# Kernel tuning notes

Measured on AMD Instinct MI355X. Metric: run time of the kernel, lower is better.

Reference implementation:

```python
import math
import jax, jax.numpy as jnp
import numpy as np

EPS = 1e-5
DIM_E = 448
DIM_H = 64
TOTAL = DIM_E + DIM_H  # 512
C = 1.0


def _project(x, c, margin=1e-3):
    sqrt_c = jnp.sqrt(c)
    norm = jnp.maximum(jnp.linalg.norm(x, axis=-1, keepdims=True), EPS)
    scale = jnp.minimum(((1.0 - margin) / sqrt_c) / norm, 1.0)
    return x * scale


def _mobius_add(x, y, c):
    x2 = jnp.sum(x * x, axis=-1, keepdims=True)
    y2 = jnp.sum(y * y, axis=-1, keepdims=True)
    xy = jnp.sum(x * y, axis=-1, keepdims=True)
    num = (1.0 + 2.0 * c * xy + c * y2) * x + (1.0 - c * x2) * y
    den = jnp.maximum(1.0 + 2.0 * c * xy + c * c * x2 * y2, EPS)
    return _project(num / den, c)


def _exp0(v, c):
    sqrt_c = jnp.sqrt(c)
    norm = jnp.maximum(jnp.linalg.norm(v, axis=-1, keepdims=True), EPS)
    return _project(jnp.tanh(sqrt_c * norm) * v / (sqrt_c * norm), c)


def _dist(x, y, c):
    # x, y broadcast to [B,S,S,dim_h]; returns [B,S,S]
    sqrt_c = jnp.sqrt(c)
    diff = _mobius_add(-x, y, c)
    norm = jnp.minimum(jnp.linalg.norm(diff, axis=-1), (1.0 - 1e-5) / sqrt_c)
    return (2.0 / sqrt_c) * jnp.arctanh(jnp.minimum(sqrt_c * norm, 1.0 - 1e-5))


def setup_inputs() -> dict:
    key = jax.random.key(0)
    ks = jax.random.split(key, 10)
    B, S = 1, 1024
    s = 1.0 / math.sqrt(TOTAL)
    inp = {
        "x": jax.random.normal(ks[0], (B, S, TOTAL), jnp.float32),
        "wq": jax.random.uniform(ks[1], (TOTAL, TOTAL), jnp.float32, -s, s),
        "bq": jax.random.uniform(ks[2], (TOTAL,), jnp.float32, -s, s),
        "wk": jax.random.uniform(ks[3], (TOTAL, TOTAL), jnp.float32, -s, s),
        "bk": jax.random.uniform(ks[4], (TOTAL,), jnp.float32, -s, s),
        "wv": jax.random.uniform(ks[5], (TOTAL, TOTAL), jnp.float32, -s, s),
        "bv": jax.random.uniform(ks[6], (TOTAL,), jnp.float32, -s, s),
        "wo": jax.random.uniform(ks[7], (TOTAL, TOTAL), jnp.float32, -s, s),
        "bo": jax.random.uniform(ks[8], (TOTAL,), jnp.float32, -s, s),
        "alpha_unconstrained": jnp.float32(0.0),
    }
    return inp


def reference(x, wq, bq, wk, bk, wv, bv, wo, bo, alpha_unconstrained):
    q = x @ wq.T + bq
    k = x @ wk.T + bk
    v = x @ wv.T + bv
    qe, qh = q[..., :DIM_E], q[..., DIM_E:]
    ke, kh = k[..., :DIM_E], k[..., DIM_E:]
    # Euclidean squared distance [B,S,S] via GEMM expansion
    qn = jnp.sum(qe * qe, axis=-1)  # [B,S]
    kn = jnp.sum(ke * ke, axis=-1)  # [B,S]
    d_e = qn[:, :, None] + kn[:, None, :] - 2.0 * jnp.einsum("bsd,btd->bst", qe, ke)
    # Hyperbolic distance on Poincare ball
    qh_h = _exp0(qh, C)
    kh_h = _exp0(kh, C)
    d_h = _dist(qh_h[:, :, None, :], kh_h[:, None, :, :], C)  # [B,S,S]
    alpha = jax.nn.softplus(alpha_unconstrained)
    dist = d_e + alpha * d_h * d_h
    logits = jnp.clip(-dist / math.sqrt(float(TOTAL)), -50.0, 0.0)
    attn = jax.nn.softmax(logits, axis=-1)
    out = jnp.einsum("bst,btd->bsd", attn, v)
    return out @ wo.T + bo
```

## Files before the change

kernel.cpp:

```cpp
#include <hip/hip_runtime.h>

#define S_LEN 1024
#define D_TOT 512
#define D_E   448

typedef short bf16x8 __attribute__((ext_vector_type(8)));
typedef float f32x4  __attribute__((ext_vector_type(4)));
typedef unsigned short u16;

__device__ __forceinline__ float frcp(float x) {
  float r; asm("v_rcp_f32 %0, %1" : "=v"(r) : "v"(x)); return r;
}

__device__ __forceinline__ float wave_sum64(float v) {
#pragma unroll
  for (int o = 32; o > 0; o >>= 1) v += __shfl_xor(v, o);
  return v;
}

__device__ __forceinline__ u16 bf16rne(float f) {
  unsigned u = __builtin_bit_cast(unsigned, f);
  return (u16)((u + 0x7fffu + ((u >> 16) & 1u)) >> 16);
}

__device__ __forceinline__ uint4 rne8(float4 a, float4 b) {
  uint4 h;
  h.x = (unsigned)bf16rne(a.x) | ((unsigned)bf16rne(a.y)<<16);
  h.y = (unsigned)bf16rne(a.z) | ((unsigned)bf16rne(a.w)<<16);
  h.z = (unsigned)bf16rne(b.x) | ((unsigned)bf16rne(b.y)<<16);
  h.w = (unsigned)bf16rne(b.z) | ((unsigned)bf16rne(b.w)<<16);
  return h;
}

#define MFMA1(ACC)                                                                              \
  _Pragma("unroll") for (int i_ = 0; i_ < 2; ++i_)                                              \
  _Pragma("unroll") for (int j_ = 0; j_ < 2; ++j_)                                              \
    ACC[i_][j_] = __builtin_amdgcn_mfma_f32_16x16x32_bf16(fAh[i_], fBh[j_], ACC[i_][j_],0,0,0);

__global__ __launch_bounds__(512,4) void qkv_mfma(
    const float* __restrict__ x,
    const float* __restrict__ wq, const float* __restrict__ bq,
    const float* __restrict__ wk, const float* __restrict__ bk,
    const float* __restrict__ wv, const float* __restrict__ bv,
    u16* __restrict__ Qch, u16* __restrict__ Kch, u16* __restrict__ vTh,
    float* __restrict__ qnpart, float* __restrict__ knpart,
    float* __restrict__ uh2a, float* __restrict__ vh2a)
{
  __shared__ __align__(16) u16 stage[2][10240];
  float* fbuf = (float*)stage;
  const int z = blockIdx.z;
  const float* W; const float* bias;
  if (z == 0)      { W = wq; bias = bq; }
  else if (z == 1) { W = wk; bias = bk; }
  else             { W = wv; bias = bv; }
  const int mBase = blockIdx.y << 6, nBase = blockIdx.x << 6;
  const int t = threadIdx.x, lane = t & 63, wave = t >> 6;
  const int kg = t >> 8, sub = t & 255;
  const int srow = sub >> 2, scol = (sub & 3) << 3;
  const int kgw = wave >> 2, wr = (wave >> 1) & 1, wc = wave & 1;

  const float* Ag = x + (size_t)(mBase + srow) * D_TOT + scol + kg * 256;
  const float* Bg = W + (size_t)(nBase + srow) * D_TOT + scol + kg * 256;

  const int sb = kg * 5120 + srow * 40 + scol;
  const int fa = kgw * 5120 + (wr * 32 + (lane & 15)) * 40 + ((lane >> 4) << 3);
  const int fb = kgw * 5120 + 2560 + (wc * 32 + (lane & 15)) * 40 + ((lane >> 4) << 3);

  float4 a0 = *(const float4*)Ag, a1 = *(const float4*)(Ag + 4);
  float4 b0 = *(const float4*)Bg, b1 = *(const float4*)(Bg + 4);
  *(uint4*)&stage[0][sb       ] = rne8(a0,a1);
  *(uint4*)&stage[0][sb + 2560] = rne8(b0,b1);
  a0 = *(const float4*)(Ag + 32); a1 = *(const float4*)(Ag + 36);
  b0 = *(const float4*)(Bg + 32); b1 = *(const float4*)(Bg + 36);

  f32x4 zero = {0.f,0.f,0.f,0.f};
  f32x4 acc[2][2] = {{zero,zero},{zero,zero}};
#pragma unroll
  for (int r = 0; r < 8; ++r) {
    __syncthreads();
    const u16* bufr = stage[r & 1];
    bf16x8 fAh[2], fBh[2];
#pragma unroll
    for (int i = 0; i < 2; ++i) {
      fAh[i] = *(const bf16x8*)&bufr[fa + i*640];
      fBh[i] = *(const bf16x8*)&bufr[fb + i*640];
    }
    if (r + 1 < 8) {
      u16* bufw = stage[(r + 1) & 1];
      *(uint4*)&bufw[sb       ] = rne8(a0,a1);
      *(uint4*)&bufw[sb + 2560] = rne8(b0,b1);
      if (r + 2 < 8) {
        const int o = (r + 2) * 32;
        a0 = *(const float4*)(Ag + o); a1 = *(const float4*)(Ag + o + 4);
        b0 = *(const float4*)(Bg + o); b1 = *(const float4*)(Bg + o + 4);
      }
    }
    MFMA1(acc);
  }

  __syncthreads();
  {
    const int r0 = wr*32 + ((lane>>4)<<2);
    const int c0 = wc*32 + (lane&15);
#pragma unroll
    for (int i = 0; i < 2; ++i)
#pragma unroll
      for (int j = 0; j < 2; ++j)
#pragma unroll
        for (int g = 0; g < 4; ++g)
          fbuf[kgw*4352 + (r0 + i*16 + g)*68 + c0 + j*16] = acc[i][j][g];
  }
  __syncthreads();
  const int erow = wave << 3;
  float val[8];
  {
    const float b = bias[nBase + lane];
#pragma unroll
    for (int r = 0; r < 8; ++r)
      val[r] = fbuf[(erow+r)*68 + lane] + fbuf[4352 + (erow+r)*68 + lane] + b;
  }

  if (z == 2) {
    u16 hh[8];
#pragma unroll
    for (int r = 0; r < 8; ++r) hh[r] = bf16rne(val[r]);
    const size_t off = (size_t)(nBase + lane) * S_LEN + mBase + erow;
    ushort4 p0{hh[0],hh[1],hh[2],hh[3]}, p1{hh[4],hh[5],hh[6],hh[7]};
    *(ushort4*)(vTh + off) = p0; *(ushort4*)(vTh + off + 4) = p1;
  } else {
    u16* Ch = z ? Kch : Qch;
    float* np_ = z ? knpart : qnpart;
    float* u2a = z ? vh2a  : uh2a;
    if (blockIdx.x < 7) {
#pragma unroll
      for (int r = 0; r < 8; ++r) {
        const int s = mBase + erow + r;
        Ch[(size_t)s*D_TOT + nBase + lane] = bf16rne(val[r]);
        float p = wave_sum64(val[r]*val[r]);
        if (lane == 0) np_[s*8 + blockIdx.x] = p;
      }
    } else {
#pragma unroll
      for (int r = 0; r < 8; ++r) {
        const int s = mBase + erow + r;
        float n2 = wave_sum64(val[r]*val[r]);
        float nn = sqrtf(n2);
        float n  = fmaxf(nn, 1e-5f);
        float e2n = __expf(2.f*n);
        float th  = 1.f - 2.f*frcp(e2n + 1.f);
        float rn  = frcp(n);
        float pn  = th * nn * rn;
        float scale = fminf(0.999f * frcp(fmaxf(pn, 1e-5f)), 1.f);
        float u = th * rn * scale * val[r];
        float un = pn * scale;
        Ch[(size_t)s*D_TOT + nBase + lane] = bf16rne(u);
        if (lane == 0) u2a[s] = un*un;
      }
    }
  }
}

__global__ __launch_bounds__(512,4) void score_mfma(
    const u16* __restrict__ Qch, const u16* __restrict__ Kch,
    const float* __restrict__ qnpart, const float* __restrict__ knpart,
    const float* __restrict__ uh2a, const float* __restrict__ vh2a,
    const float* __restrict__ alpha_u,
    u16* __restrict__ Eh, float* __restrict__ rowpart)
{
  __shared__ __align__(16) char shm_[69632];
  __shared__ float rowscal[256];
  u16* stg = (u16*)shm_;
  float* fbuf = (float*)shm_;
  const int t = threadIdx.x, lane = t & 63, wave = t >> 6;
  const int mBase = blockIdx.y << 6, nBase = blockIdx.x << 6;
  if (t < 64) {
    float s_ = 0.f;
#pragma unroll
    for (int c = 0; c < 7; ++c) s_ += qnpart[(mBase+t)*8 + c];
    rowscal[t] = s_;
  } else if (t < 128) {
    float s_ = 0.f;
#pragma unroll
    for (int c = 0; c < 7; ++c) s_ += knpart[(nBase+t-64)*8 + c];
    rowscal[t] = s_;
  } else if (t < 192) rowscal[t] = uh2a[mBase + t - 128];
  else if (t < 256)   rowscal[t] = vh2a[nBase + t - 192];

  const int kg = t >> 8, sub = t & 255;
  const int srow = sub >> 2, scol = (sub & 3) << 3;
  const int kgw = wave >> 2, wr = (wave >> 1) & 1, wc = wave & 1;
  const u16* Agh = Qch + (size_t)(mBase+srow)*D_TOT + scol;
  const u16* Bgh = Kch + (size_t)(nBase+srow)*D_TOT + scol;

  const int sb  = kg * 5120 + srow * 40 + scol;
  const int fa  = kgw * 5120 + (wr * 32 + (lane & 15)) * 40 + ((lane >> 4) << 3);
  const int fbh = kgw * 5120 + 2560 + (wc * 32 + (lane & 15)) * 40 + ((lane >> 4) << 3);

  int kb = kg * 224;
  uint4 rAh = *(const uint4*)(Agh + kb);
  uint4 rBh = *(const uint4*)(Bgh + kb);
  *(uint4*)&stg[sb       ] = rAh;
  *(uint4*)&stg[sb + 2560] = rBh;
  kb = kg * 224 + 32;
  rAh = *(const uint4*)(Agh + kb);
  rBh = *(const uint4*)(Bgh + kb);

  f32x4 zero = {0.f,0.f,0.f,0.f};
  f32x4 accE[2][2] = {{zero,zero},{zero,zero}};
  f32x4 accH[2][2] = {{zero,zero},{zero,zero}};
#pragma unroll
  for (int r = 0; r < 8; ++r) {
    __syncthreads();
    const u16* bufr = stg + (r & 1) * 10240;
    bf16x8 fAh[2], fBh[2];
#pragma unroll
    for (int i = 0; i < 2; ++i) {
      fAh[i] = *(const bf16x8*)&bufr[fa  + i*640];
      fBh[i] = *(const bf16x8*)&bufr[fbh + i*640];
    }
    if (r + 1 < 8) {
      u16* bufw = stg + ((r + 1) & 1) * 10240;
      *(uint4*)&bufw[sb       ] = rAh;
      *(uint4*)&bufw[sb + 2560] = rBh;
      if (r + 2 < 8) {
        const int o = (r + 2 < 7) ? (kg*224 + (r+2)*32) : (448 + kg*32);
        rAh = *(const uint4*)(Agh + o);
        rBh = *(const uint4*)(Bgh + o);
      }
    }
    if (r < 7) { MFMA1(accE) } else { MFMA1(accH) }
  }

  __syncthreads();
  {
    const int r0 = wr*32 + ((lane>>4)<<2);
    const int c0 = wc*32 + (lane&15);
#pragma unroll
    for (int i = 0; i < 2; ++i)
#pragma unroll
      for (int j = 0; j < 2; ++j)
#pragma unroll
        for (int g = 0; g < 4; ++g) {
          fbuf[       kgw*4352 + (r0 + i*16 + g)*68 + c0 + j*16] = accE[i][j][g];
          fbuf[8704 + kgw*4352 + (r0 + i*16 + g)*68 + c0 + j*16] = accH[i][j][g];
        }
  }
  __syncthreads();
  const int erow = wave << 3;
  float eE[8], eH[8];
#pragma unroll
  for (int r = 0; r < 8; ++r) {
    eE[r] = fbuf[(erow+r)*68 + lane] + fbuf[4352 + (erow+r)*68 + lane];
    eH[r] = fbuf[8704 + (erow+r)*68 + lane] + fbuf[8704 + 4352 + (erow+r)*68 + lane];
  }

  const float alpha = __logf(1.f + __expf(alpha_u[0]));
  const float inv_s = 0.04419417382415922f;
  const float knl = rowscal[64 + lane], v2 = rowscal[192 + lane];
#pragma unroll
  for (int r = 0; r < 8; ++r) {
    const int s = mBase + erow + r;
    const float qns = rowscal[erow + r], u2 = rowscal[128 + erow + r];
    float de   = qns + knl - 2.f * eE[r];
    float dH   = eH[r];
    float Ac   = 1.f - 2.f*dH + v2;
    float Bc   = 1.f - u2;
    float num2 = Ac*Ac*u2 + Bc*Bc*v2 - 2.f*Ac*Bc*dH;
    float den  = fmaxf(1.f - 2.f*dH + u2*v2, 1e-5f);
    float frac = sqrtf(fmaxf(num2, 0.f)) * frcp(den);
    float nrm  = fminf(frac, 0.999f);
    float dh_  = __logf((1.f + nrm) * frcp(1.f - nrm));
    float dist = de + alpha * dh_ * dh_;
    float lg   = fminf(fmaxf(-dist * inv_s, -50.f), 0.f);
    float e    = __expf(lg);
    Eh[(size_t)s*S_LEN + nBase + lane] = bf16rne(e);
    float rs = wave_sum64(e);
    if (lane == 0) rowpart[s*16 + blockIdx.x] = rs;
  }
}

__global__ __launch_bounds__(512,4) void av_mfma(
    const u16* __restrict__ Eh, const u16* __restrict__ vTh,
    const float* __restrict__ rowpart,
    u16* __restrict__ out1h)
{
  __shared__ __align__(16) u16 stage[2][15360];
  __shared__ float rinvl[32];
  float* fbuf = (float*)stage;
  const int t = threadIdx.x, lane = t & 63, wave = t >> 6;
  const int mBase = blockIdx.y << 5, nBase = blockIdx.x << 6;
  if (t < 32) {
    float s_ = 0.f;
#pragma unroll
    for (int c = 0; c < 16; ++c) s_ += rowpart[(mBase+t)*16 + c];
    rinvl[t] = 1.f / s_;
  }
  const int kg = t >> 7, sub = t & 127;
  const int arow = sub >> 2, acol = (sub & 3) << 3;
  const int brow0 = sub >> 2, brow1 = 32 + (sub >> 2), bcol = (sub & 3) << 3;
  const int kgw = wave >> 1, wc = wave & 1;

  const u16* Ag = Eh  + (size_t)(mBase+arow)*S_LEN + kg*256 + acol;
  const u16* B0 = vTh + (size_t)(nBase+brow0)*S_LEN + kg*256 + bcol;
  const u16* B1 = vTh + (size_t)(nBase+brow1)*S_LEN + kg*256 + bcol;

  const int sA  = kg*3840 + arow*40 + acol;
  const int sB0 = kg*3840 + 1280 + brow0*40 + bcol;
  const int sB1 = kg*3840 + 1280 + brow1*40 + bcol;
  const int fa  = kgw*3840 + (lane&15)*40 + ((lane>>4)<<3);
  const int fb  = kgw*3840 + 1280 + (wc*32 + (lane&15))*40 + ((lane>>4)<<3);

  uint4 rA = *(const uint4*)Ag;
  uint4 rb0 = *(const uint4*)B0, rb1 = *(const uint4*)B1;
  *(uint4*)&stage[0][sA ] = rA;
  *(uint4*)&stage[0][sB0] = rb0; *(uint4*)&stage[0][sB1] = rb1;
  rA = *(const uint4*)(Ag + 32);
  rb0 = *(const uint4*)(B0 + 32); rb1 = *(const uint4*)(B1 + 32);

  f32x4 zero = {0.f,0.f,0.f,0.f};
  f32x4 acc[2][2] = {{zero,zero},{zero,zero}};
#pragma unroll
  for (int r = 0; r < 8; ++r) {
    __syncthreads();
    const u16* bufr = stage[r & 1];
    bf16x8 fAh[2], fBh[2];
#pragma unroll
    for (int i = 0; i < 2; ++i) {
      fAh[i] = *(const bf16x8*)&bufr[fa + i*640];
      fBh[i] = *(const bf16x8*)&bufr[fb + i*640];
    }
    if (r + 1 < 8) {
      u16* bufw = stage[(r + 1) & 1];
      *(uint4*)&bufw[sA ] = rA;
      *(uint4*)&bufw[sB0] = rb0; *(uint4*)&bufw[sB1] = rb1;
      if (r + 2 < 8) {
        const int o = (r + 2) * 32;
        rA = *(const uint4*)(Ag + o);
        rb0 = *(const uint4*)(B0 + o); rb1 = *(const uint4*)(B1 + o);
      }
    }
    MFMA1(acc);
  }

  __syncthreads();
  {
    const int r0 = (lane>>4)<<2;
    const int c0 = wc*32 + (lane&15);
#pragma unroll
    for (int i = 0; i < 2; ++i)
#pragma unroll
      for (int j = 0; j < 2; ++j)
#pragma unroll
        for (int g = 0; g < 4; ++g)
          fbuf[kgw*2176 + (r0 + i*16 + g)*68 + c0 + j*16] = acc[i][j][g];
  }
  __syncthreads();
  const int erow = wave << 2;
#pragma unroll
  for (int r = 0; r < 4; ++r) {
    const int row = erow + r;
    float e = fbuf[row*68 + lane] + fbuf[2176 + row*68 + lane]
            + fbuf[4352 + row*68 + lane] + fbuf[6528 + row*68 + lane];
    float v_ = e * rinvl[row];
    const int s = mBase + row;
    out1h[(size_t)s*D_TOT + nBase + lane] = bf16rne(v_);
  }
}

__global__ __launch_bounds__(512,4) void final_mfma(
    const u16* __restrict__ out1h,
    const float* __restrict__ wo, const float* __restrict__ bo,
    float* __restrict__ out)
{
  __shared__ __align__(16) u16 stage[2][15360];
  float* fbuf = (float*)stage;
  const int t = threadIdx.x, lane = t & 63, wave = t >> 6;
  const int mBase = blockIdx.y << 5, nBase = blockIdx.x << 6;
  const int kg = t >> 7, sub = t & 127;
  const int arow = sub >> 2, acol = (sub & 3) << 3;
  const int brow0 = sub >> 2, brow1 = 32 + (sub >> 2), bcol = (sub & 3) << 3;
  const int kgw = wave >> 1, wc = wave & 1;

  const u16*   Ag = out1h + (size_t)(mBase+arow)*D_TOT + kg*128 + acol;
  const float* B0 = wo + (size_t)(nBase+brow0)*D_TOT + kg*128 + bcol;
  const float* B1 = wo + (size_t)(nBase+brow1)*D_TOT + kg*128 + bcol;

  const int sA  = kg*3840 + arow*40 + acol;
  const int sB0 = kg*3840 + 1280 + brow0*40 + bcol;
  const int sB1 = kg*3840 + 1280 + brow1*40 + bcol;
  const int fa  = kgw*3840 + (lane&15)*40 + ((lane>>4)<<3);
  const int fb  = kgw*3840 + 1280 + (wc*32 + (lane&15))*40 + ((lane>>4)<<3);

  uint4 rA = *(const uint4*)Ag;
  float4 b00 = *(const float4*)B0, b01 = *(const float4*)(B0 + 4);
  float4 b10 = *(const float4*)B1, b11 = *(const float4*)(B1 + 4);
  *(uint4*)&stage[0][sA ] = rA;
  *(uint4*)&stage[0][sB0] = rne8(b00,b01);
  *(uint4*)&stage[0][sB1] = rne8(b10,b11);
  rA = *(const uint4*)(Ag + 32);
  b00 = *(const float4*)(B0 + 32); b01 = *(const float4*)(B0 + 36);
  b10 = *(const float4*)(B1 + 32); b11 = *(const float4*)(B1 + 36);

  f32x4 zero = {0.f,0.f,0.f,0.f};
  f32x4 acc[2][2] = {{zero,zero},{zero,zero}};
#pragma unroll
  for (int r = 0; r < 4; ++r) {
    __syncthreads();
    const u16* bufr = stage[r & 1];
    bf16x8 fAh[2], fBh[2];
#pragma unroll
    for (int i = 0; i < 2; ++i) {
      fAh[i] = *(const bf16x8*)&bufr[fa + i*640];
      fBh[i] = *(const bf16x8*)&bufr[fb + i*640];
    }
    if (r + 1 < 4) {
      u16* bufw = stage[(r + 1) & 1];
      *(uint4*)&bufw[sA ] = rA;
      *(uint4*)&bufw[sB0] = rne8(b00,b01);
      *(uint4*)&bufw[sB1] = rne8(b10,b11);
      if (r + 2 < 4) {
        const int o = (r + 2) * 32;
        rA = *(const uint4*)(Ag + o);
        b00 = *(const float4*)(B0 + o); b01 = *(const float4*)(B0 + o + 4);
        b10 = *(const float4*)(B1 + o); b11 = *(const float4*)(B1 + o + 4);
      }
    }
    MFMA1(acc);
  }

  __syncthreads();
  {
    const int r0 = (lane>>4)<<2;
    const int c0 = wc*32 + (lane&15);
#pragma unroll
    for (int i = 0; i < 2; ++i)
#pragma unroll
      for (int j = 0; j < 2; ++j)
#pragma unroll
        for (int g = 0; g < 4; ++g)
          fbuf[kgw*2176 + (r0 + i*16 + g)*68 + c0 + j*16] = acc[i][j][g];
  }
  __syncthreads();
  const int erow = wave << 2;
  const float b = bo[nBase + lane];
#pragma unroll
  for (int r = 0; r < 4; ++r) {
    const int row = erow + r;
    float e = fbuf[row*68 + lane] + fbuf[2176 + row*68 + lane]
            + fbuf[4352 + row*68 + lane] + fbuf[6528 + row*68 + lane];
    out[(size_t)(mBase+row)*D_TOT + nBase + lane] = e + b;
  }
}

extern "C" void kernel_launch(void* const* d_in, const int* in_sizes, int n_in,
                              void* d_out, int out_size, void* d_ws, size_t ws_size,
                              hipStream_t stream)
{
  const float* x   = (const float*)d_in[0];
  const float* wq  = (const float*)d_in[1];
  const float* bq  = (const float*)d_in[2];
  const float* wk  = (const float*)d_in[3];
  const float* bk  = (const float*)d_in[4];
  const float* wv  = (const float*)d_in[5];
  const float* bv  = (const float*)d_in[6];
  const float* wo  = (const float*)d_in[7];
  const float* bo  = (const float*)d_in[8];
  const float* alpha_u = (const float*)d_in[9];
  float* out = (float*)d_out;

  u16* U = (u16*)d_ws;
  u16* Qch   = U + 0;
  u16* Kch   = U + 524288;
  u16* vTh   = U + 1048576;
  u16* Eh    = U + 1572864;
  u16* out1h = U + 2621440;
  float* F = (float*)(U + 3145728);
  float* qnpart  = F;
  float* knpart  = F + 8192;
  float* uh2a    = F + 16384;
  float* vh2a    = F + 17408;
  float* rowpart = F + 18432;

  qkv_mfma<<<dim3(8,16,3), 512, 0, stream>>>(x, wq,bq, wk,bk, wv,bv,
      Qch, Kch, vTh, qnpart, knpart, uh2a, vh2a);
  score_mfma<<<dim3(16,16), 512, 0, stream>>>(Qch, Kch,
      qnpart, knpart, uh2a, vh2a, alpha_u, Eh, rowpart);
  av_mfma<<<dim3(8,32), 512, 0, stream>>>(Eh, vTh, rowpart, out1h);
  final_mfma<<<dim3(8,32), 512, 0, stream>>>(out1h, wo, bo, out);
}
```

Before: 34.59 us.

## Move V projection into score kernel to balance grid and overlap work

```diff
diff --git a/kernel.cpp b/kernel.cpp
--- a/kernel.cpp
+++ b/kernel.cpp
@@ -37,22 +37,19 @@
   _Pragma("unroll") for (int j_ = 0; j_ < 2; ++j_)                                              \
     ACC[i_][j_] = __builtin_amdgcn_mfma_f32_16x16x32_bf16(fAh[i_], fBh[j_], ACC[i_][j_],0,0,0);
 
-__global__ __launch_bounds__(512,4) void qkv_mfma(
+__global__ __launch_bounds__(512,4) void qk_mfma(
     const float* __restrict__ x,
     const float* __restrict__ wq, const float* __restrict__ bq,
     const float* __restrict__ wk, const float* __restrict__ bk,
-    const float* __restrict__ wv, const float* __restrict__ bv,
-    u16* __restrict__ Qch, u16* __restrict__ Kch, u16* __restrict__ vTh,
+    u16* __restrict__ Qch, u16* __restrict__ Kch,
     float* __restrict__ qnpart, float* __restrict__ knpart,
     float* __restrict__ uh2a, float* __restrict__ vh2a)
 {
   __shared__ __align__(16) u16 stage[2][10240];
   float* fbuf = (float*)stage;
   const int z = blockIdx.z;
-  const float* W; const float* bias;
-  if (z == 0)      { W = wq; bias = bq; }
-  else if (z == 1) { W = wk; bias = bk; }
-  else             { W = wv; bias = bv; }
+  const float* W    = z ? wk : wq;
+  const float* bias = z ? bk : bq;
   const int mBase = blockIdx.y << 6, nBase = blockIdx.x << 6;
   const int t = threadIdx.x, lane = t & 63, wave = t >> 6;
   const int kg = t >> 8, sub = t & 255;
@@ -120,162 +117,228 @@
       val[r] = fbuf[(erow+r)*68 + lane] + fbuf[4352 + (erow+r)*68 + lane] + b;
   }
 
-  if (z == 2) {
-    u16 hh[8];
-#pragma unroll
-    for (int r = 0; r < 8; ++r) hh[r] = bf16rne(val[r]);
-    const size_t off = (size_t)(nBase + lane) * S_LEN + mBase + erow;
-    ushort4 p0{hh[0],hh[1],hh[2],hh[3]}, p1{hh[4],hh[5],hh[6],hh[7]};
-    *(ushort4*)(vTh + off) = p0; *(ushort4*)(vTh + off + 4) = p1;
+  u16* Ch = z ? Kch : Qch;
+  float* np_ = z ? knpart : qnpart;
+  float* u2a = z ? vh2a  : uh2a;
+  if (blockIdx.x < 7) {
+#pragma unroll
+    for (int r = 0; r < 8; ++r) {
+      const int s = mBase + erow + r;
+      Ch[(size_t)s*D_TOT + nBase + lane] = bf16rne(val[r]);
+      float p = wave_sum64(val[r]*val[r]);
+      if (lane == 0) np_[s*8 + blockIdx.x] = p;
+    }
   } else {
-    u16* Ch = z ? Kch : Qch;
-    float* np_ = z ? knpart : qnpart;
-    float* u2a = z ? vh2a  : uh2a;
-    if (blockIdx.x < 7) {
-#pragma unroll
-      for (int r = 0; r < 8; ++r) {
-        const int s = mBase + erow + r;
-        Ch[(size_t)s*D_TOT + nBase + lane] = bf16rne(val[r]);
-        float p = wave_sum64(val[r]*val[r]);
-        if (lane == 0) np_[s*8 + blockIdx.x] = p;
-      }
-    } else {
-#pragma unroll
-      for (int r = 0; r < 8; ++r) {
-        const int s = mBase + erow + r;
-        float n2 = wave_sum64(val[r]*val[r]);
-        float nn = sqrtf(n2);
-        float n  = fmaxf(nn, 1e-5f);
-        float e2n = __expf(2.f*n);
-        float th  = 1.f - 2.f*frcp(e2n + 1.f);
-        float rn  = frcp(n);
-        float pn  = th * nn * rn;
-        float scale = fminf(0.999f * frcp(fmaxf(pn, 1e-5f)), 1.f);
-        float u = th * rn * scale * val[r];
-        float un = pn * scale;
-        Ch[(size_t)s*D_TOT + nBase + lane] = bf16rne(u);
-        if (lane == 0) u2a[s] = un*un;
-      }
-    }
-  }
-}
-
-__global__ __launch_bounds__(512,4) void score_mfma(
+#pragma unroll
+    for (int r = 0; r < 8; ++r) {
+      const int s = mBase + erow + r;
+      float n2 = wave_sum64(val[r]*val[r]);
+      float nn = sqrtf(n2);
+      float n  = fmaxf(nn, 1e-5f);
+      float e2n = __expf(2.f*n);
+      float th  = 1.f - 2.f*frcp(e2n + 1.f);
+      float rn  = frcp(n);
+      float pn  = th * nn * rn;
+      float scale = fminf(0.999f * frcp(fmaxf(pn, 1e-5f)), 1.f);
+      float u = th * rn * scale * val[r];
+      float un = pn * scale;
+      Ch[(size_t)s*D_TOT + nBase + lane] = bf16rne(u);
+      if (lane == 0) u2a[s] = un*un;
+    }
+  }
+}
+
+__global__ __launch_bounds__(512,4) void score_v(
     const u16* __restrict__ Qch, const u16* __restrict__ Kch,
     const float* __restrict__ qnpart, const float* __restrict__ knpart,
     const float* __restrict__ uh2a, const float* __restrict__ vh2a,
     const float* __restrict__ alpha_u,
-    u16* __restrict__ Eh, float* __restrict__ rowpart)
+    const float* __restrict__ x,
+    const float* __restrict__ wv, const float* __restrict__ bv,
+    u16* __restrict__ Eh, float* __restrict__ rowpart,
+    u16* __restrict__ vTh)
 {
   __shared__ __align__(16) char shm_[69632];
   __shared__ float rowscal[256];
   u16* stg = (u16*)shm_;
   float* fbuf = (float*)shm_;
+  const int bid = blockIdx.x;
   const int t = threadIdx.x, lane = t & 63, wave = t >> 6;
-  const int mBase = blockIdx.y << 6, nBase = blockIdx.x << 6;
-  if (t < 64) {
-    float s_ = 0.f;
-#pragma unroll
-    for (int c = 0; c < 7; ++c) s_ += qnpart[(mBase+t)*8 + c];
-    rowscal[t] = s_;
-  } else if (t < 128) {
-    float s_ = 0.f;
-#pragma unroll
-    for (int c = 0; c < 7; ++c) s_ += knpart[(nBase+t-64)*8 + c];
-    rowscal[t] = s_;
-  } else if (t < 192) rowscal[t] = uh2a[mBase + t - 128];
-  else if (t < 256)   rowscal[t] = vh2a[nBase + t - 192];
-
   const int kg = t >> 8, sub = t & 255;
   const int srow = sub >> 2, scol = (sub & 3) << 3;
   const int kgw = wave >> 2, wr = (wave >> 1) & 1, wc = wave & 1;
-  const u16* Agh = Qch + (size_t)(mBase+srow)*D_TOT + scol;
-  const u16* Bgh = Kch + (size_t)(nBase+srow)*D_TOT + scol;
-
-  const int sb  = kg * 5120 + srow * 40 + scol;
-  const int fa  = kgw * 5120 + (wr * 32 + (lane & 15)) * 40 + ((lane >> 4) << 3);
-  const int fbh = kgw * 5120 + 2560 + (wc * 32 + (lane & 15)) * 40 + ((lane >> 4) << 3);
-
-  int kb = kg * 224;
-  uint4 rAh = *(const uint4*)(Agh + kb);
-  uint4 rBh = *(const uint4*)(Bgh + kb);
-  *(uint4*)&stg[sb       ] = rAh;
-  *(uint4*)&stg[sb + 2560] = rBh;
-  kb = kg * 224 + 32;
-  rAh = *(const uint4*)(Agh + kb);
-  rBh = *(const uint4*)(Bgh + kb);
-
-  f32x4 zero = {0.f,0.f,0.f,0.f};
-  f32x4 accE[2][2] = {{zero,zero},{zero,zero}};
-  f32x4 accH[2][2] = {{zero,zero},{zero,zero}};
-#pragma unroll
-  for (int r = 0; r < 8; ++r) {
-    __syncthreads();
-    const u16* bufr = stg + (r & 1) * 10240;
-    bf16x8 fAh[2], fBh[2];
-#pragma unroll
-    for (int i = 0; i < 2; ++i) {
-      fAh[i] = *(const bf16x8*)&bufr[fa  + i*640];
-      fBh[i] = *(const bf16x8*)&bufr[fbh + i*640];
-    }
-    if (r + 1 < 8) {
-      u16* bufw = stg + ((r + 1) & 1) * 10240;
-      *(uint4*)&bufw[sb       ] = rAh;
-      *(uint4*)&bufw[sb + 2560] = rBh;
-      if (r + 2 < 8) {
-        const int o = (r + 2 < 7) ? (kg*224 + (r+2)*32) : (448 + kg*32);
-        rAh = *(const uint4*)(Agh + o);
-        rBh = *(const uint4*)(Bgh + o);
-      }
-    }
-    if (r < 7) { MFMA1(accE) } else { MFMA1(accH) }
-  }
-
-  __syncthreads();
-  {
-    const int r0 = wr*32 + ((lane>>4)<<2);
-    const int c0 = wc*32 + (lane&15);
-#pragma unroll
-    for (int i = 0; i < 2; ++i)
-#pragma unroll
-      for (int j = 0; j < 2; ++j)
-#pragma unroll
-        for (int g = 0; g < 4; ++g) {
-          fbuf[       kgw*4352 + (r0 + i*16 + g)*68 + c0 + j*16] = accE[i][j][g];
-          fbuf[8704 + kgw*4352 + (r0 + i*16 + g)*68 + c0 + j*16] = accH[i][j][g];
+
+  if (bid < 256) {
+    const int nx = bid & 15;
+    const int mBase = (bid >> 4) << 6, nBase = nx << 6;
+    if (t < 64) {
+      float s_ = 0.f;
+#pragma unroll
+      for (int c = 0; c < 7; ++c) s_ += qnpart[(mBase+t)*8 + c];
+      rowscal[t] = s_;
+    } else if (t < 128) {
+      float s_ = 0.f;
+#pragma unroll
+      for (int c = 0; c < 7; ++c) s_ += knpart[(nBase+t-64)*8 + c];
+      rowscal[t] = s_;
+    } else if (t < 192) rowscal[t] = uh2a[mBase + t - 128];
+    else if (t < 256)   rowscal[t] = vh2a[nBase + t - 192];
+
+    const u16* Agh = Qch + (size_t)(mBase+srow)*D_TOT + scol;
+    const u16* Bgh = Kch + (size_t)(nBase+srow)*D_TOT + scol;
+
+    const int sb  = kg * 5120 + srow * 40 + scol;
+    const int fa  = kgw * 5120 + (wr * 32 + (lane & 15)) * 40 + ((lane >> 4) << 3);
+    const int fbh = kgw * 5120 + 2560 + (wc * 32 + (lane & 15)) * 40 + ((lane >> 4) << 3);
+
+    int kb = kg * 224;
+    uint4 rAh = *(const uint4*)(Agh + kb);
+    uint4 rBh = *(const uint4*)(Bgh + kb);
+    *(uint4*)&stg[sb       ] = rAh;
+    *(uint4*)&stg[sb + 2560] = rBh;
+    kb = kg * 224 + 32;
+    rAh = *(const uint4*)(Agh + kb);
+    rBh = *(const uint4*)(Bgh + kb);
+
+    f32x4 zero = {0.f,0.f,0.f,0.f};
+    f32x4 accE[2][2] = {{zero,zero},{zero,zero}};
+    f32x4 accH[2][2] = {{zero,zero},{zero,zero}};
+#pragma unroll
+    for (int r = 0; r < 8; ++r) {
+      __syncthreads();
+      const u16* bufr = stg + (r & 1) * 10240;
+      bf16x8 fAh[2], fBh[2];
+#pragma unroll
+      for (int i = 0; i < 2; ++i) {
+        fAh[i] = *(const bf16x8*)&bufr[fa  + i*640];
+        fBh[i] = *(const bf16x8*)&bufr[fbh + i*640];
+      }
+      if (r + 1 < 8) {
+        u16* bufw = stg + ((r + 1) & 1) * 10240;
+        *(uint4*)&bufw[sb       ] = rAh;
+        *(uint4*)&bufw[sb + 2560] = rBh;
+        if (r + 2 < 8) {
+          const int o = (r + 2 < 7) ? (kg*224 + (r+2)*32) : (448 + kg*32);
+          rAh = *(const uint4*)(Agh + o);
+          rBh = *(const uint4*)(Bgh + o);
         }
-  }
-  __syncthreads();
-  const int erow = wave << 3;
-  float eE[8], eH[8];
-#pragma unroll
-  for (int r = 0; r < 8; ++r) {
-    eE[r] = fbuf[(erow+r)*68 + lane] + fbuf[4352 + (erow+r)*68 + lane];
-    eH[r] = fbuf[8704 + (erow+r)*68 + lane] + fbuf[8704 + 4352 + (erow+r)*68 + lane];
-  }
-
-  const float alpha = __logf(1.f + __expf(alpha_u[0]));
-  const float inv_s = 0.04419417382415922f;
-  const float knl = rowscal[64 + lane], v2 = rowscal[192 + lane];
-#pragma unroll
-  for (int r = 0; r < 8; ++r) {
-    const int s = mBase + erow + r;
-    const float qns = rowscal[erow + r], u2 = rowscal[128 + erow + r];
-    float de   = qns + knl - 2.f * eE[r];
-    float dH   = eH[r];
-    float Ac   = 1.f - 2.f*dH + v2;
-    float Bc   = 1.f - u2;
-    float num2 = Ac*Ac*u2 + Bc*Bc*v2 - 2.f*Ac*Bc*dH;
-    float den  = fmaxf(1.f - 2.f*dH + u2*v2, 1e-5f);
-    float frac = sqrtf(fmaxf(num2, 0.f)) * frcp(den);
-    float nrm  = fminf(frac, 0.999f);
-    float dh_  = __logf((1.f + nrm) * frcp(1.f - nrm));
-    float dist = de + alpha * dh_ * dh_;
-    float lg   = fminf(fmaxf(-dist * inv_s, -50.f), 0.f);
-    float e    = __expf(lg);
-    Eh[(size_t)s*S_LEN + nBase + lane] = bf16rne(e);
-    float rs = wave_sum64(e);
-    if (lane == 0) rowpart[s*16 + blockIdx.x] = rs;
+      }
+      if (r < 7) { MFMA1(accE) } else { MFMA1(accH) }
+    }
+
+    __syncthreads();
+    {
+      const int r0 = wr*32 + ((lane>>4)<<2);
+      const int c0 = wc*32 + (lane&15);
+#pragma unroll
+      for (int i = 0; i < 2; ++i)
+#pragma unroll
+        for (int j = 0; j < 2; ++j)
+#pragma unroll
+          for (int g = 0; g < 4; ++g) {
+            fbuf[       kgw*4352 + (r0 + i*16 + g)*68 + c0 + j*16] = accE[i][j][g];
+            fbuf[8704 + kgw*4352 + (r0 + i*16 + g)*68 + c0 + j*16] = accH[i][j][g];
+          }
+    }
+    __syncthreads();
+    const int erow = wave << 3;
+    float eE[8], eH[8];
+#pragma unroll
+    for (int r = 0; r < 8; ++r) {
+      eE[r] = fbuf[(erow+r)*68 + lane] + fbuf[4352 + (erow+r)*68 + lane];
+      eH[r] = fbuf[8704 + (erow+r)*68 + lane] + fbuf[8704 + 4352 + (erow+r)*68 + lane];
+    }
+
+    const float alpha = __logf(1.f + __expf(alpha_u[0]));
+    const float inv_s = 0.04419417382415922f;
+    const float knl = rowscal[64 + lane], v2 = rowscal[192 + lane];
+#pragma unroll
+    for (int r = 0; r < 8; ++r) {
+      const int s = mBase + erow + r;
+      const float qns = rowscal[erow + r], u2 = rowscal[128 + erow + r];
+      float de   = qns + knl - 2.f * eE[r];
+      float dH   = eH[r];
+      float Ac   = 1.f - 2.f*dH + v2;
+      float Bc   = 1.f - u2;
+      float num2 = Ac*Ac*u2 + Bc*Bc*v2 - 2.f*Ac*Bc*dH;
+      float den  = fmaxf(1.f - 2.f*dH + u2*v2, 1e-5f);
+      float frac = sqrtf(fmaxf(num2, 0.f)) * frcp(den);
+      float nrm  = fminf(frac, 0.999f);
+      float dh_  = __logf((1.f + nrm) * frcp(1.f - nrm));
+      float dist = de + alpha * dh_ * dh_;
+      float lg   = fminf(fmaxf(-dist * inv_s, -50.f), 0.f);
+      float e    = __expf(lg);
+      Eh[(size_t)s*S_LEN + nBase + lane] = bf16rne(e);
+      float rs = wave_sum64(e);
+      if (lane == 0) rowpart[s*16 + nx] = rs;
+    }
+  } else {
+    const int b2 = bid - 256;
+    const int mBase = (b2 >> 3) << 6, nBase = (b2 & 7) << 6;
+
+    const float* Ag = x  + (size_t)(mBase + srow) * D_TOT + scol + kg * 256;
+    const float* Bg = wv + (size_t)(nBase + srow) * D_TOT + scol + kg * 256;
+
+    const int sb = kg * 5120 + srow * 40 + scol;
+    const int fa = kgw * 5120 + (wr * 32 + (lane & 15)) * 40 + ((lane >> 4) << 3);
+    const int fb = kgw * 5120 + 2560 + (wc * 32 + (lane & 15)) * 40 + ((lane >> 4) << 3);
+
+    float4 a0 = *(const float4*)Ag, a1 = *(const float4*)(Ag + 4);
+    float4 b0 = *(const float4*)Bg, b1 = *(const float4*)(Bg + 4);
+    *(uint4*)&stg[sb       ] = rne8(a0,a1);
+    *(uint4*)&stg[sb + 2560] = rne8(b0,b1);
+    a0 = *(const float4*)(Ag + 32); a1 = *(const float4*)(Ag + 36);
+    b0 = *(const float4*)(Bg + 32); b1 = *(const float4*)(Bg + 36);
+
+    f32x4 zero = {0.f,0.f,0.f,0.f};
+    f32x4 acc[2][2] = {{zero,zero},{zero,zero}};
+#pragma unroll
+    for (int r = 0; r < 8; ++r) {
+      __syncthreads();
+      const u16* bufr = stg + (r & 1) * 10240;
+      bf16x8 fAh[2], fBh[2];
+#pragma unroll
+      for (int i = 0; i < 2; ++i) {
+        fAh[i] = *(const bf16x8*)&bufr[fa + i*640];
+        fBh[i] = *(const bf16x8*)&bufr[fb + i*640];
+      }
+      if (r + 1 < 8) {
+        u16* bufw = stg + ((r + 1) & 1) * 10240;
+        *(uint4*)&bufw[sb       ] = rne8(a0,a1);
+        *(uint4*)&bufw[sb + 2560] = rne8(b0,b1);
+        if (r + 2 < 8) {
+          const int o = (r + 2) * 32;
+          a0 = *(const float4*)(Ag + o); a1 = *(const float4*)(Ag + o + 4);
+          b0 = *(const float4*)(Bg + o); b1 = *(const float4*)(Bg + o + 4);
+        }
+      }
+      MFMA1(acc);
+    }
+
+    __syncthreads();
+    {
+      const int r0 = wr*32 + ((lane>>4)<<2);
+      const int c0 = wc*32 + (lane&15);
+#pragma unroll
+      for (int i = 0; i < 2; ++i)
+#pragma unroll
+        for (int j = 0; j < 2; ++j)
+#pragma unroll
+          for (int g = 0; g < 4; ++g)
+            fbuf[kgw*4352 + (r0 + i*16 + g)*68 + c0 + j*16] = acc[i][j][g];
+    }
+    __syncthreads();
+    const int erow = wave << 3;
+    u16 hh[8];
+    {
+      const float b = bv[nBase + lane];
+#pragma unroll
+      for (int r = 0; r < 8; ++r)
+        hh[r] = bf16rne(fbuf[(erow+r)*68 + lane] + fbuf[4352 + (erow+r)*68 + lane] + b);
+    }
+    const size_t off = (size_t)(nBase + lane) * S_LEN + mBase + erow;
+    ushort4 p0{hh[0],hh[1],hh[2],hh[3]}, p1{hh[4],hh[5],hh[6],hh[7]};
+    *(ushort4*)(vTh + off) = p0; *(ushort4*)(vTh + off + 4) = p1;
   }
 }
 
@@ -481,10 +544,10 @@
   float* vh2a    = F + 17408;
   float* rowpart = F + 18432;
 
-  qkv_mfma<<<dim3(8,16,3), 512, 0, stream>>>(x, wq,bq, wk,bk, wv,bv,
-      Qch, Kch, vTh, qnpart, knpart, uh2a, vh2a);
-  score_mfma<<<dim3(16,16), 512, 0, stream>>>(Qch, Kch,
-      qnpart, knpart, uh2a, vh2a, alpha_u, Eh, rowpart);
+  qk_mfma<<<dim3(8,16,2), 512, 0, stream>>>(x, wq,bq, wk,bk,
+      Qch, Kch, qnpart, knpart, uh2a, vh2a);
+  score_v<<<dim3(384), 512, 0, stream>>>(Qch, Kch,
+      qnpart, knpart, uh2a, vh2a, alpha_u, x, wv, bv, Eh, rowpart, vTh);
   av_mfma<<<dim3(8,32), 512, 0, stream>>>(Eh, vTh, rowpart, out1h);
   final_mfma<<<dim3(8,32), 512, 0, stream>>>(out1h, wo, bo, out);
 }
```

Result: slower. 35.76 us (+3.4%).
